# Optimization experiments

Hardware: AMD Instinct MI355X
Metric: run time of the kernel (lower is better)

The kernel has to match this reference:

```python
import jax, jax.numpy as jnp
import numpy as np

N, E, F_IN, H, D, C = 50000, 800000, 128, 4, 64, 40
HD = H * D
NEG_SLOPE = 0.2


def setup_inputs() -> dict:
    key = jax.random.key(0)
    ks = jax.random.split(key, 16)
    x = jax.random.normal(ks[0], (N, F_IN), dtype=jnp.float32)
    edge_index = jax.random.randint(ks[1], (2, E), 0, N, dtype=jnp.int64)
    def glorot(k, shape):
        fan = shape[0] + shape[-1]
        return jax.random.normal(k, shape, dtype=jnp.float32) * jnp.sqrt(2.0 / fan)
    params = {
        'W1': glorot(ks[2], (F_IN, HD)), 'as1': glorot(ks[3], (H, D)), 'ad1': glorot(ks[4], (H, D)), 'b1': jnp.zeros((HD,), jnp.float32),
        'W2': glorot(ks[5], (HD, HD)),   'as2': glorot(ks[6], (H, D)), 'ad2': glorot(ks[7], (H, D)), 'b2': jnp.zeros((HD,), jnp.float32),
        'W3': glorot(ks[8], (HD, HD)),   'as3': glorot(ks[9], (H, D)), 'ad3': glorot(ks[10], (H, D)), 'b3': jnp.zeros((HD,), jnp.float32),
        'Wl': glorot(ks[11], (HD, C)),   'bl': jnp.zeros((C,), jnp.float32),
    }
    return {'x': x, 'edge_index': edge_index, **params}


def gat_layer(x, src, dst, W, a_src, a_dst, b):
    # x: [N, F] -> h: [N, H, D]
    h = (x @ W).reshape(N, H, D)
    alpha_s = jnp.sum(h * a_src, axis=-1)  # [N, H]
    alpha_d = jnp.sum(h * a_dst, axis=-1)  # [N, H]
    e = alpha_s[src] + alpha_d[dst]        # [E', H]
    e = jnp.where(e > 0, e, NEG_SLOPE * e)  # leaky_relu
    # segment softmax over destination nodes
    m = jax.ops.segment_max(e, dst, num_segments=N)  # [N, H]
    m = jnp.where(jnp.isfinite(m), m, 0.0)
    ex = jnp.exp(e - m[dst])
    s = jax.ops.segment_sum(ex, dst, num_segments=N)  # [N, H]
    att = ex / (s[dst] + 1e-16)                        # [E', H]
    # weighted scatter-aggregate of source features
    out = jax.ops.segment_sum(h[src] * att[:, :, None], dst, num_segments=N)  # [N, H, D]
    return out.reshape(N, HD) + b


def reference(x, edge_index, W1, as1, ad1, b1, W2, as2, ad2, b2, W3, as3, ad3, b3, Wl, bl):
    # PyG GATConv adds self-loops by default
    loops = jnp.arange(N, dtype=edge_index.dtype)
    src = jnp.concatenate([edge_index[0], loops])
    dst = jnp.concatenate([edge_index[1], loops])
    # dropout is identity in eval mode
    h = jax.nn.elu(gat_layer(x, src, dst, W1, as1, ad1, b1))
    h = jax.nn.elu(gat_layer(h, src, dst, W2, as2, ad2, b2))
    h = jax.nn.elu(gat_layer(h, src, dst, W3, as3, ad3, b3))
    logits = h @ Wl + bl
    return jax.nn.log_softmax(logits, axis=1)
```

## Files before the change

kernel.cpp:

```cpp
#include <hip/hip_runtime.h>
#include <math.h>

#define NN 50000
#define NE 800000
#define ET (NE + NN)
#define FIN 128
#define HDIM 256
#define NHEAD 4
#define NCLS 40
#define NEG 0.2f
#define NB_SCAN ((NN + 255) / 256)

typedef short bf16x8 __attribute__((ext_vector_type(8)));
typedef float f32x4 __attribute__((ext_vector_type(4)));

__device__ __forceinline__ unsigned short f2b(float f) {
    unsigned int u = __float_as_uint(f);
    unsigned int r = (u + 0x7fffu + ((u >> 16) & 1u)) >> 16;
    return (unsigned short)r;
}
__device__ __forceinline__ unsigned int cvtpk(float lo, float hi) {
    unsigned int r;
    asm volatile("v_cvt_pk_bf16_f32 %0, %1, %2" : "=v"(r) : "v"(lo), "v"(hi));
    return r;
}
__device__ __forceinline__ float b2f(unsigned short u) {
    unsigned int x = ((unsigned int)u) << 16;
    return __uint_as_float(x);
}

__global__ void detect_kernel(const int* __restrict__ ei32, int* __restrict__ flag) {
    int lane = threadIdx.x;
    int nz = ei32[1 + 2 * lane] | ei32[129 + 2 * lane];
    unsigned long long b = __ballot(nz != 0);
    if (lane == 0) *flag = (b == 0ull) ? 1 : 0;
}

__device__ __forceinline__ int load_node(const int* ei32, int is64, long long idx) {
    return is64 ? ei32[2 * idx] : ei32[idx];
}

__global__ void deg_kernel(const int* __restrict__ ei32, const int* __restrict__ flag,
                           int* __restrict__ deg) {
    int e = blockIdx.x * blockDim.x + threadIdx.x;
    if (e >= ET) return;
    int is64 = *flag;
    int d = (e < NE) ? load_node(ei32, is64, (long long)NE + e) : (e - NE);
    atomicAdd(&deg[d], 1);
}

__global__ void scan1(const int* __restrict__ deg, int* __restrict__ incl,
                      int* __restrict__ bsum) {
    __shared__ int sm[256];
    int i = blockIdx.x * 256 + threadIdx.x;
    int v = (i < NN) ? deg[i] : 0;
    sm[threadIdx.x] = v;
    __syncthreads();
    for (int o = 1; o < 256; o <<= 1) {
        int add = (threadIdx.x >= o) ? sm[threadIdx.x - o] : 0;
        __syncthreads();
        sm[threadIdx.x] += add;
        __syncthreads();
    }
    if (i < NN) incl[i] = sm[threadIdx.x];
    if (threadIdx.x == 255) bsum[blockIdx.x] = sm[255];
}

__global__ void scan2(int* __restrict__ bsum) {
    __shared__ int sm[256];
    int t = threadIdx.x;
    sm[t] = (t < NB_SCAN) ? bsum[t] : 0;
    __syncthreads();
    if (t == 0) {
        int run = 0;
        for (int b = 0; b < NB_SCAN; b++) { int v = sm[b]; sm[b] = run; run += v; }
    }
    __syncthreads();
    if (t < NB_SCAN) bsum[t] = sm[t];
}

__global__ void scan3(const int* __restrict__ incl, const int* __restrict__ bsum,
                      const int* __restrict__ deg, int* __restrict__ indptr,
                      int* __restrict__ cursor) {
    int i = blockIdx.x * 256 + threadIdx.x;
    if (i < NN) {
        int v = bsum[blockIdx.x] + incl[i];
        indptr[i + 1] = v;
        cursor[i] = v - deg[i];
    }
    if (i == 0) indptr[0] = 0;
}

__global__ void fill_kernel(const int* __restrict__ ei32, const int* __restrict__ flag,
                            int* __restrict__ cursor, int* __restrict__ esrc) {
    int e = blockIdx.x * blockDim.x + threadIdx.x;
    if (e >= ET) return;
    int is64 = *flag;
    int s, d;
    if (e < NE) {
        s = load_node(ei32, is64, (long long)e);
        d = load_node(ei32, is64, (long long)NE + e);
    } else {
        s = d = e - NE;
    }
    int pos = atomicAdd(&cursor[d], 1);
    esrc[pos] = s;
}

__global__ __launch_bounds__(256) void conv_kernel(const float* __restrict__ in,
                                                   unsigned short* __restrict__ out, int n) {
    int i = (blockIdx.x * 256 + threadIdx.x) * 8;
    if (i + 8 > n) return;
    float4 f0 = *(const float4*)(in + i);
    float4 f1 = *(const float4*)(in + i + 4);
    uint4 pk;
    pk.x = cvtpk(f0.x, f0.y);
    pk.y = cvtpk(f0.z, f0.w);
    pk.z = cvtpk(f1.x, f1.y);
    pk.w = cvtpk(f1.z, f1.w);
    *(uint4*)(out + i) = pk;
}

__global__ __launch_bounds__(256) void wconv3_kernel(const float* __restrict__ W1,
                                                     const float* __restrict__ W2,
                                                     const float* __restrict__ W3,
                                                     unsigned short* __restrict__ Wt1,
                                                     unsigned short* __restrict__ Wt2,
                                                     unsigned short* __restrict__ Wt3) {
    __shared__ float sm[32][33];
    int z = blockIdx.z;
    const float* W = (z == 0) ? W1 : (z == 1) ? W2 : W3;
    unsigned short* Wt = (z == 0) ? Wt1 : (z == 1) ? Wt2 : Wt3;
    int K = (z == 0) ? FIN : HDIM;
    int k0 = blockIdx.y * 32;
    if (k0 >= K) return;
    int tx = threadIdx.x & 31, ty = threadIdx.x >> 5;
    int n0 = blockIdx.x * 32;
#pragma unroll
    for (int j = 0; j < 4; j++)
        sm[ty + j * 8][tx] = W[(size_t)(k0 + ty + j * 8) * HDIM + n0 + tx];
    __syncthreads();
#pragma unroll
    for (int j = 0; j < 4; j++)
        Wt[(size_t)(n0 + ty + j * 8) * K + k0 + tx] = f2b(sm[tx][ty + j * 8]);
}

__global__ __launch_bounds__(256) void gemm_mfma(const unsigned short* __restrict__ A,
                                                 const unsigned short* __restrict__ Bt,
                                                 unsigned short* __restrict__ Cb,
                                                 const float* __restrict__ a_s,
                                                 const float* __restrict__ a_d,
                                                 float* __restrict__ als,
                                                 float* __restrict__ ald,
                                                 int M, int K) {
    __shared__ unsigned short As[128][72];
    __shared__ unsigned short Bs[64][72];
    int bid = blockIdx.x;
    int xcd = bid & 7, g = bid >> 3;
    int cblk = g & 3, rg = g >> 2;
    int rblk = rg * 8 + xcd;
    int r0 = rblk * 128, n0 = cblk * 64;
    if (r0 >= M) return;

    int t = threadIdx.x;
    int lane = t & 63, wid = t >> 6;

    f32x4 acc[2][4];
#pragma unroll
    for (int m = 0; m < 2; m++)
#pragma unroll
        for (int n = 0; n < 4; n++)
            acc[m][n] = (f32x4){0.f, 0.f, 0.f, 0.f};

    int ar = t >> 1, ah = (t & 1) * 32;
    int arow = r0 + ar; if (arow > M - 1) arow = M - 1;
    const unsigned short* ga = A + (size_t)arow * K + ah;
    int bn = t >> 2, bq = (t & 3) * 16;
    const unsigned short* gb = Bt + (size_t)(n0 + bn) * K + bq;

    int fr = lane & 15;
    int kf = (lane >> 4) * 8;

    for (int k0 = 0; k0 < K; k0 += 64) {
#pragma unroll
        for (int j = 0; j < 4; j++)
            *(uint4*)&As[ar][ah + j * 8] = *(const uint4*)(ga + k0 + j * 8);
#pragma unroll
        for (int j = 0; j < 2; j++)
            *(uint4*)&Bs[bn][bq + j * 8] = *(const uint4*)(gb + k0 + j * 8);
        __syncthreads();
#pragma unroll
        for (int kk = 0; kk < 64; kk += 32) {
            bf16x8 a[2], b[4];
#pragma unroll
            for (int m = 0; m < 2; m++)
                a[m] = *(const bf16x8*)&As[wid * 32 + m * 16 + fr][kk + kf];
#pragma unroll
            for (int n = 0; n < 4; n++)
                b[n] = *(const bf16x8*)&Bs[n * 16 + fr][kk + kf];
#pragma unroll
            for (int m = 0; m < 2; m++)
#pragma unroll
                for (int n = 0; n < 4; n++)
                    acc[m][n] = __builtin_amdgcn_mfma_f32_16x16x32_bf16(a[m], b[n], acc[m][n], 0, 0, 0);
        }
        __syncthreads();
    }

    int rbase = r0 + wid * 32 + (lane >> 4) * 4;
    int cbase = n0 + fr;
    int head = n0 >> 6;
    float asv[4], adv[4];
#pragma unroll
    for (int n = 0; n < 4; n++) {
        asv[n] = a_s[cbase + n * 16];
        adv[n] = a_d[cbase + n * 16];
    }
#pragma unroll
    for (int m = 0; m < 2; m++)
#pragma unroll
        for (int q = 0; q < 4; q++) {
            int gr = rbase + m * 16 + q;
            float vs = 0.f, vd = 0.f;
#pragma unroll
            for (int n = 0; n < 4; n++) {
                float v = acc[m][n][q];
                vs += v * asv[n];
                vd += v * adv[n];
            }
#pragma unroll
            for (int o = 8; o > 0; o >>= 1) {
                vs += __shfl_xor(vs, o);
                vd += __shfl_xor(vd, o);
            }
            if (fr == 0 && gr < M) {
                als[gr * NHEAD + head] = vs;
                ald[gr * NHEAD + head] = vd;
            }
        }

    unsigned short (*Cs)[68] = (unsigned short(*)[68])&As[0][0];
    int lr0 = wid * 32 + (lane >> 4) * 4;
#pragma unroll
    for (int m = 0; m < 2; m++)
#pragma unroll
        for (int q = 0; q < 4; q++)
#pragma unroll
            for (int n = 0; n < 4; n++)
                Cs[lr0 + m * 16 + q][fr + n * 16] = f2b(acc[m][n][q]);
    __syncthreads();
    int tr = t >> 4;
    int tc = (t & 15) * 4;
#pragma unroll
    for (int rr = 0; rr < 8; rr++) {
        int lr = tr + rr * 16;
        int gr = r0 + lr;
        if (gr < M) *(ushort4*)(Cb + (size_t)gr * HDIM + n0 + tc) = *(const ushort4*)&Cs[lr][tc];
    }
}

__global__ __launch_bounds__(256) void agg_kernel(const unsigned short* __restrict__ projb,
                                                  const float* __restrict__ als,
                                                  const float* __restrict__ ald,
                                                  const int* __restrict__ indptr,
                                                  const int* __restrict__ esrc,
                                                  const float* __restrict__ bias,
                                                  unsigned short* __restrict__ featb) {
    int wid = threadIdx.x >> 6;
    int v = blockIdx.x * 4 + wid;
    if (v >= NN) return;
    int lane = threadIdx.x & 63;
    int h = lane >> 4;
    int sub = lane & 15;
    int beg = indptr[v], end = indptr[v + 1];
    float adv = ald[v * NHEAD + h];

    float e0 = 0.f, e1 = 0.f;
    int s0r = 0, s1r = 0;
    float m = -INFINITY, ss = 0.f;
    int idx = 0;
    for (int i = beg + sub; i < end; i += 16, idx++) {
        int s = esrc[i];
        float e = als[s * NHEAD + h] + adv;
        e = e > 0.f ? e : NEG * e;
        if (idx == 0) { e0 = e; s0r = s; }
        else if (idx == 1) { e1 = e; s1r = s; }
        if (e > m) {
            ss = ss * __expf(m - e) + 1.f;
            m = e;
        } else {
            ss += __expf(e - m);
        }
    }
#pragma unroll
    for (int o = 8; o > 0; o >>= 1) {
        float m2 = __shfl_xor(m, o);
        float s2 = __shfl_xor(ss, o);
        float mn = fmaxf(m, m2);
        float a = (m == mn) ? ss : ss * __expf(m - mn);
        float b = (m2 == mn) ? s2 : s2 * __expf(m2 - mn);
        m = mn;
        ss = a + b;
    }
    float inv = 1.f / (ss + 1e-16f);

    float4 acc = make_float4(0.f, 0.f, 0.f, 0.f);
    int chunk = 0;
    for (int c = beg; c < end; c += 16, chunk++) {
        int rem = end - c;
        int sreg;
        float eC;
        if (chunk == 0) { sreg = s0r; eC = e0; }
        else if (chunk == 1) { sreg = s1r; eC = e1; }
        else {
            int i = c + (sub < rem ? sub : rem - 1);
            sreg = esrc[i];
            eC = als[sreg * NHEAD + h] + adv;
            eC = eC > 0.f ? eC : NEG * eC;
        }
        float wreg = (sub < rem) ? __expf(eC - m) * inv : 0.f;

        ushort4 p[16];
#pragma unroll
        for (int j = 0; j < 16; j++) {
            int s = __shfl(sreg, j);
            p[j] = *(const ushort4*)(projb + (size_t)s * HDIM + (lane << 2));
        }
#pragma unroll
        for (int j = 0; j < 16; j++) {
            float w = __shfl(wreg, (h << 4) | j);
            acc.x += b2f(p[j].x) * w;
            acc.y += b2f(p[j].y) * w;
            acc.z += b2f(p[j].z) * w;
            acc.w += b2f(p[j].w) * w;
        }
    }

    const float4 b4 = *(const float4*)(bias + (lane << 2));
    float4 r;
    r.x = acc.x + b4.x;
    r.y = acc.y + b4.y;
    r.z = acc.z + b4.z;
    r.w = acc.w + b4.w;
    r.x = r.x > 0.f ? r.x : __expf(r.x) - 1.f;
    r.y = r.y > 0.f ? r.y : __expf(r.y) - 1.f;
    r.z = r.z > 0.f ? r.z : __expf(r.z) - 1.f;
    r.w = r.w > 0.f ? r.w : __expf(r.w) - 1.f;
    uint2 o2;
    o2.x = cvtpk(r.x, r.y);
    o2.y = cvtpk(r.z, r.w);
    *(uint2*)(featb + (size_t)v * HDIM + (lane << 2)) = o2;
}

__global__ __launch_bounds__(256) void final_kernel(const unsigned short* __restrict__ featb,
                                                    const float* __restrict__ Wl,
                                                    const float* __restrict__ bl,
                                                    float* __restrict__ out) {
    const int BK = 16;
    __shared__ float As[BK][65];
    __shared__ float Bs[BK][65];
    int tx = threadIdx.x & 15, ty = threadIdx.x >> 4;
    int row0 = blockIdx.x * 64;
    float acc[4][4] = {};
    for (int k0 = 0; k0 < HDIM; k0 += BK) {
#pragma unroll
        for (int i = 0; i < 4; i++) {
            int l = threadIdx.x + 256 * i;
            int r = l >> 4, c = l & 15;
            int gr = row0 + r;
            float v = 0.f;
            if (gr < NN) v = b2f(featb[(size_t)gr * HDIM + k0 + c]);
            As[c][r] = v;
        }
#pragma unroll
        for (int i = 0; i < 4; i++) {
            int l = threadIdx.x + 256 * i;
            int r = l >> 6, c = l & 63;
            Bs[r][c] = (c < NCLS) ? Wl[(size_t)(k0 + r) * NCLS + c] : 0.f;
        }
        __syncthreads();
#pragma unroll
        for (int k = 0; k < BK; k++) {
            float a[4], b[4];
#pragma unroll
            for (int i = 0; i < 4; i++) a[i] = As[k][ty + 16 * i];
#pragma unroll
            for (int j = 0; j < 4; j++) b[j] = Bs[k][tx + 16 * j];
#pragma unroll
            for (int i = 0; i < 4; i++)
#pragma unroll
                for (int j = 0; j < 4; j++) acc[i][j] += a[i] * b[j];
        }
        __syncthreads();
    }
    float b0 = bl[tx], b1 = bl[tx + 16], b2 = (tx < 8) ? bl[tx + 32] : 0.f;
#pragma unroll
    for (int i = 0; i < 4; i++) {
        int gr = row0 + ty + 16 * i;
        if (gr >= NN) continue;
        float l0 = acc[i][0] + b0;
        float l1 = acc[i][1] + b1;
        float l2 = (tx < 8) ? acc[i][2] + b2 : -INFINITY;
        float m = fmaxf(fmaxf(l0, l1), l2);
#pragma unroll
        for (int o = 8; o > 0; o >>= 1) m = fmaxf(m, __shfl_xor(m, o));
        float s = __expf(l0 - m) + __expf(l1 - m) + ((tx < 8) ? __expf(l2 - m) : 0.f);
#pragma unroll
        for (int o = 8; o > 0; o >>= 1) s += __shfl_xor(s, o);
        float lse = m + __logf(s);
        out[(size_t)gr * NCLS + tx] = l0 - lse;
        out[(size_t)gr * NCLS + tx + 16] = l1 - lse;
        if (tx < 8) out[(size_t)gr * NCLS + tx + 32] = l2 - lse;
    }
}

extern "C" void kernel_launch(void* const* d_in, const int* in_sizes, int n_in,
                              void* d_out, int out_size, void* d_ws, size_t ws_size,
                              hipStream_t stream) {
    const float* x  = (const float*)d_in[0];
    const int* ei32 = (const int*)d_in[1];
    const float* W1 = (const float*)d_in[2];
    const float* as1 = (const float*)d_in[3];
    const float* ad1 = (const float*)d_in[4];
    const float* b1 = (const float*)d_in[5];
    const float* W2 = (const float*)d_in[6];
    const float* as2 = (const float*)d_in[7];
    const float* ad2 = (const float*)d_in[8];
    const float* b2 = (const float*)d_in[9];
    const float* W3 = (const float*)d_in[10];
    const float* as3 = (const float*)d_in[11];
    const float* ad3 = (const float*)d_in[12];
    const float* b3 = (const float*)d_in[13];
    const float* Wl = (const float*)d_in[14];
    const float* bl = (const float*)d_in[15];
    float* out = (float*)d_out;

    char* w = (char*)d_ws;
    unsigned short* projb = (unsigned short*)w;  w += (size_t)NN * HDIM * 2;
    unsigned short* featb = (unsigned short*)w;  w += (size_t)NN * HDIM * 2;
    unsigned short* xb    = (unsigned short*)w;  w += (size_t)NN * FIN * 2;
    unsigned short* Wt1b  = (unsigned short*)w;  w += (size_t)HDIM * FIN * 2;
    unsigned short* Wt2b  = (unsigned short*)w;  w += (size_t)HDIM * HDIM * 2;
    unsigned short* Wt3b  = (unsigned short*)w;  w += (size_t)HDIM * HDIM * 2;
    float* als  = (float*)w;  w += (size_t)NN * NHEAD * 4;
    float* ald  = (float*)w;  w += (size_t)NN * NHEAD * 4;
    int* deg    = (int*)w;    w += (size_t)NN * 4;
    int* incl   = (int*)w;    w += (size_t)NN * 4;
    int* bsum   = (int*)w;    w += 256 * 4;
    int* indptr = (int*)w;    w += (size_t)(NN + 1) * 4;
    int* cursor = (int*)w;    w += (size_t)NN * 4;
    int* esrc   = (int*)w;    w += (size_t)ET * 4;
    int* flag   = (int*)w;    w += 64;

    conv_kernel<<<(NN * FIN / 8 + 255) / 256, 256, 0, stream>>>(x, xb, NN * FIN);
    wconv3_kernel<<<dim3(8, 8, 3), 256, 0, stream>>>(W1, W2, W3, Wt1b, Wt2b, Wt3b);

    hipMemsetAsync(deg, 0, (size_t)NN * 4, stream);
    detect_kernel<<<1, 64, 0, stream>>>(ei32, flag);
    deg_kernel<<<(ET + 255) / 256, 256, 0, stream>>>(ei32, flag, deg);
    scan1<<<NB_SCAN, 256, 0, stream>>>(deg, incl, bsum);
    scan2<<<1, 256, 0, stream>>>(bsum);
    scan3<<<NB_SCAN, 256, 0, stream>>>(incl, bsum, deg, indptr, cursor);
    fill_kernel<<<(ET + 255) / 256, 256, 0, stream>>>(ei32, flag, cursor, esrc);

    int ggrid = 8 * 4 * (((NN + 127) / 128 + 7) / 8);
    int agrid = (NN + 3) / 4;

    gemm_mfma<<<ggrid, 256, 0, stream>>>(xb, Wt1b, projb, as1, ad1, als, ald, NN, FIN);
    agg_kernel<<<agrid, 256, 0, stream>>>(projb, als, ald, indptr, esrc, b1, featb);
    gemm_mfma<<<ggrid, 256, 0, stream>>>(featb, Wt2b, projb, as2, ad2, als, ald, NN, HDIM);
    agg_kernel<<<agrid, 256, 0, stream>>>(projb, als, ald, indptr, esrc, b2, featb);
    gemm_mfma<<<ggrid, 256, 0, stream>>>(featb, Wt3b, projb, as3, ad3, als, ald, NN, HDIM);
    agg_kernel<<<agrid, 256, 0, stream>>>(projb, als, ald, indptr, esrc, b3, featb);
    final_kernel<<<(NN + 63) / 64, 256, 0, stream>>>(featb, Wl, bl, out);
}
```

Baseline: 410.6 us.

## Unroll aggregation loop over two edge chunks and inline int64 index detection

The aggregation loop now processes two 16-edge chunks per iteration and issues all 32 gathered feature loads before any accumulation, so more memory requests are in flight at once. The separate detect kernel is removed. Each block of the degree and fill kernels now detects int32 versus int64 indices itself through a shared-memory flag, which saves one launch. In exchange the unrolled loop uses more registers, which may lower occupancy, and every block repeats a small detection read.

Result: no change. 406.0 us (-1.1%).

```diff
diff --git a/kernel.cpp b/kernel.cpp
--- a/kernel.cpp
+++ b/kernel.cpp
@@ -29,22 +29,25 @@
     return __uint_as_float(x);
 }
 
-__global__ void detect_kernel(const int* __restrict__ ei32, int* __restrict__ flag) {
-    int lane = threadIdx.x;
-    int nz = ei32[1 + 2 * lane] | ei32[129 + 2 * lane];
-    unsigned long long b = __ballot(nz != 0);
-    if (lane == 0) *flag = (b == 0ull) ? 1 : 0;
+__device__ __forceinline__ int sniff_is64(const int* __restrict__ ei32, int* s64p) {
+    if (threadIdx.x < 64) {
+        int nz = ei32[1 + 2 * threadIdx.x] | ei32[129 + 2 * threadIdx.x];
+        unsigned long long b = __ballot(nz != 0);
+        if (threadIdx.x == 0) *s64p = (b == 0ull) ? 1 : 0;
+    }
+    __syncthreads();
+    return *s64p;
 }
 
 __device__ __forceinline__ int load_node(const int* ei32, int is64, long long idx) {
     return is64 ? ei32[2 * idx] : ei32[idx];
 }
 
-__global__ void deg_kernel(const int* __restrict__ ei32, const int* __restrict__ flag,
-                           int* __restrict__ deg) {
+__global__ void deg_kernel(const int* __restrict__ ei32, int* __restrict__ deg) {
+    __shared__ int s64;
+    int is64 = sniff_is64(ei32, &s64);
     int e = blockIdx.x * blockDim.x + threadIdx.x;
     if (e >= ET) return;
-    int is64 = *flag;
     int d = (e < NE) ? load_node(ei32, is64, (long long)NE + e) : (e - NE);
     atomicAdd(&deg[d], 1);
 }
@@ -91,11 +94,12 @@
     if (i == 0) indptr[0] = 0;
 }
 
-__global__ void fill_kernel(const int* __restrict__ ei32, const int* __restrict__ flag,
+__global__ void fill_kernel(const int* __restrict__ ei32,
                             int* __restrict__ cursor, int* __restrict__ esrc) {
+    __shared__ int s64;
+    int is64 = sniff_is64(ei32, &s64);
     int e = blockIdx.x * blockDim.x + threadIdx.x;
     if (e >= ET) return;
-    int is64 = *flag;
     int s, d;
     if (e < NE) {
         s = load_node(ei32, is64, (long long)e);
@@ -305,30 +309,77 @@
     float inv = 1.f / (ss + 1e-16f);
 
     float4 acc = make_float4(0.f, 0.f, 0.f, 0.f);
+    int c = beg;
     int chunk = 0;
-    for (int c = beg; c < end; c += 16, chunk++) {
+    for (; c + 16 < end; c += 32, chunk += 2) {
+        int remB = end - (c + 16); if (remB > 16) remB = 16;
+        int sA, sB;
+        float eA, eB;
+        if (chunk == 0) {
+            sA = s0r; eA = e0;
+            sB = s1r; eB = e1;
+        } else {
+            sA = esrc[c + sub];
+            eA = als[sA * NHEAD + h] + adv;
+            eA = eA > 0.f ? eA : NEG * eA;
+            int iB = c + 16 + (sub < remB ? sub : remB - 1);
+            sB = esrc[iB];
+            eB = als[sB * NHEAD + h] + adv;
+            eB = eB > 0.f ? eB : NEG * eB;
+        }
+        float wA = __expf(eA - m) * inv;
+        float wB = (sub < remB) ? __expf(eB - m) * inv : 0.f;
+
+        ushort4 pA[16], pB[16];
+#pragma unroll
+        for (int j = 0; j < 16; j++) {
+            int s = __shfl(sA, j);
+            pA[j] = *(const ushort4*)(projb + (size_t)s * HDIM + (lane << 2));
+        }
+#pragma unroll
+        for (int j = 0; j < 16; j++) {
+            int s = __shfl(sB, j);
+            pB[j] = *(const ushort4*)(projb + (size_t)s * HDIM + (lane << 2));
+        }
+#pragma unroll
+        for (int j = 0; j < 16; j++) {
+            float w = __shfl(wA, (h << 4) | j);
+            acc.x += b2f(pA[j].x) * w;
+            acc.y += b2f(pA[j].y) * w;
+            acc.z += b2f(pA[j].z) * w;
+            acc.w += b2f(pA[j].w) * w;
+        }
+#pragma unroll
+        for (int j = 0; j < 16; j++) {
+            float w = __shfl(wB, (h << 4) | j);
+            acc.x += b2f(pB[j].x) * w;
+            acc.y += b2f(pB[j].y) * w;
+            acc.z += b2f(pB[j].z) * w;
+            acc.w += b2f(pB[j].w) * w;
+        }
+    }
+    if (c < end) {
         int rem = end - c;
-        int sreg;
-        float eC;
-        if (chunk == 0) { sreg = s0r; eC = e0; }
-        else if (chunk == 1) { sreg = s1r; eC = e1; }
+        int sA;
+        float eA;
+        if (chunk == 0) { sA = s0r; eA = e0; }
+        else if (chunk == 1) { sA = s1r; eA = e1; }
         else {
             int i = c + (sub < rem ? sub : rem - 1);
-            sreg = esrc[i];
-            eC = als[sreg * NHEAD + h] + adv;
-            eC = eC > 0.f ? eC : NEG * eC;
-        }
-        float wreg = (sub < rem) ? __expf(eC - m) * inv : 0.f;
-
+            sA = esrc[i];
+            eA = als[sA * NHEAD + h] + adv;
+            eA = eA > 0.f ? eA : NEG * eA;
+        }
+        float wA = (sub < rem) ? __expf(eA - m) * inv : 0.f;
         ushort4 p[16];
 #pragma unroll
         for (int j = 0; j < 16; j++) {
-            int s = __shfl(sreg, j);
+            int s = __shfl(sA, j);
             p[j] = *(const ushort4*)(projb + (size_t)s * HDIM + (lane << 2));
         }
 #pragma unroll
         for (int j = 0; j < 16; j++) {
-            float w = __shfl(wreg, (h << 4) | j);
+            float w = __shfl(wA, (h << 4) | j);
             acc.x += b2f(p[j].x) * w;
             acc.y += b2f(p[j].y) * w;
             acc.z += b2f(p[j].z) * w;
@@ -450,18 +501,16 @@
     int* indptr = (int*)w;    w += (size_t)(NN + 1) * 4;
     int* cursor = (int*)w;    w += (size_t)NN * 4;
     int* esrc   = (int*)w;    w += (size_t)ET * 4;
-    int* flag   = (int*)w;    w += 64;
 
     conv_kernel<<<(NN * FIN / 8 + 255) / 256, 256, 0, stream>>>(x, xb, NN * FIN);
     wconv3_kernel<<<dim3(8, 8, 3), 256, 0, stream>>>(W1, W2, W3, Wt1b, Wt2b, Wt3b);
 
     hipMemsetAsync(deg, 0, (size_t)NN * 4, stream);
-    detect_kernel<<<1, 64, 0, stream>>>(ei32, flag);
-    deg_kernel<<<(ET + 255) / 256, 256, 0, stream>>>(ei32, flag, deg);
+    deg_kernel<<<(ET + 255) / 256, 256, 0, stream>>>(ei32, deg);
     scan1<<<NB_SCAN, 256, 0, stream>>>(deg, incl, bsum);
     scan2<<<1, 256, 0, stream>>>(bsum);
     scan3<<<NB_SCAN, 256, 0, stream>>>(incl, bsum, deg, indptr, cursor);
-    fill_kernel<<<(ET + 255) / 256, 256, 0, stream>>>(ei32, flag, cursor, esrc);
+    fill_kernel<<<(ET + 255) / 256, 256, 0, stream>>>(ei32, cursor, esrc);
 
     int ggrid = 8 * 4 * (((NN + 127) / 128 + 7) / 8);
     int agrid = (NN + 3) / 4;
```
